# Kernel tuning notes

Hardware: AMD Instinct MI355X
Metric: run time of the kernel (lower is better)

## Reference

```python
import jax, jax.numpy as jnp
import numpy as np

DECAY = 0.8
CODEBOOK_SIZE = 1024
DIM = 128


def setup_inputs() -> dict:
    key = jax.random.key(0)
    k1, k2 = jax.random.split(key)
    x = jax.random.normal(k1, (16, 4096, DIM), dtype=jnp.float32)
    embed = jax.random.normal(k2, (CODEBOOK_SIZE, DIM), dtype=jnp.float32)
    ema_embed = embed * 1.0  # ema_num_initial = 1.0
    ema_num = jnp.ones((CODEBOOK_SIZE,), dtype=jnp.float32)
    return {"x": x, "embed": embed, "ema_embed": ema_embed, "ema_num": ema_num}


def reference(x, embed, ema_embed, ema_num):
    # flatten: [..., d] -> [N, d]
    shape = x.shape
    flatten = x.reshape(-1, shape[-1])  # [N, d]
    distance = -2.0 * (flatten @ embed.T) + jnp.sum(embed * embed, axis=-1)  # [N, K]
    embed_ind = jnp.argmin(distance, axis=-1)  # [N]
    quantize = embed[embed_ind.reshape(shape[:-1])]  # gather -> [..., d]

    # training branch: onehot^T @ flatten == segment_sum over code indices
    num_curr = jax.ops.segment_sum(
        jnp.ones_like(embed_ind, dtype=jnp.float32), embed_ind,
        num_segments=CODEBOOK_SIZE)  # [K]
    embed_curr = jax.ops.segment_sum(
        flatten.astype(jnp.float32), embed_ind,
        num_segments=CODEBOOK_SIZE)  # [K, d]

    ema_num_new = ema_num * DECAY + (1.0 - DECAY) * num_curr
    ema_embed_new = ema_embed * DECAY + (1.0 - DECAY) * embed_curr
    embed_new = ema_embed_new / ema_num_new[:, None]
    return quantize, embed_new, ema_embed_new, ema_num_new
```

## Files before the change

### kernel.cpp

```cpp
#include <hip/hip_runtime.h>

#define NPTS    65536
#define DIM     128
#define KCODES  1024
#define BM      128
#define TILE_C  64
#define NTHR    256
#define QUART_C 256
#define NTILE   (QUART_C / TILE_C)

typedef _Float16 f16x8 __attribute__((ext_vector_type(8)));
typedef float    f32x4 __attribute__((ext_vector_type(4)));

__device__ __forceinline__ void gload_lds16(const void* g, void* l) {
    __builtin_amdgcn_global_load_lds(
        (const __attribute__((address_space(1))) void*)g,
        (__attribute__((address_space(3))) void*)l, 16, 0, 0);
}
__device__ __forceinline__ unsigned mono32(float f) {
    unsigned u = __builtin_bit_cast(unsigned, f);
    return (u & 0x80000000u) ? ~u : (u | 0x80000000u);
}

__global__ __launch_bounds__(256)
void pack_kernel(const float* __restrict__ embed, _Float16* __restrict__ ebf,
                 int* __restrict__ ghist, int* __restrict__ gcursor,
                 const float* __restrict__ ema_embed, float* __restrict__ acc,
                 float* __restrict__ hn, unsigned long long* __restrict__ kmax)
{
    __shared__ float partial[256];
    const int t = threadIdx.x;
    const int b = blockIdx.x;
    const int g = b * 256 + t;
    if (g < KCODES) { ghist[g] = 0; gcursor[g] = 0; }
    {
        float4 e0 = reinterpret_cast<const float4*>(ema_embed)[g];
        float4 e1 = reinterpret_cast<const float4*>(ema_embed)[g + 16384];
        reinterpret_cast<float4*>(acc)[g] =
            (float4){0.8f * e0.x, 0.8f * e0.y, 0.8f * e0.z, 0.8f * e0.w};
        reinterpret_cast<float4*>(acc)[g + 16384] =
            (float4){0.8f * e1.x, 0.8f * e1.y, 0.8f * e1.z, 0.8f * e1.w};
    }
    #pragma unroll
    for (int k = 0; k < 4; ++k) kmax[g * 4 + k] = 0ull;

    const int tc  = g >> 10;
    const int f   = (g >> 6) & 15;
    const int l   = g & 63;
    const int nt  = f >> 2;
    const int akk = f & 3;
    const int hg  = l >> 4;
    const int n   = l & 15;
    const int c   = tc * TILE_C + nt * 16 + n;
    const int d0  = akk * 32 + hg * 8;
    const float* src = embed + (long)c * DIM + d0;
    float4 v0 = *reinterpret_cast<const float4*>(src);
    float4 v1 = *reinterpret_cast<const float4*>(src + 4);
    float vv[8] = {v0.x, v0.y, v0.z, v0.w, v1.x, v1.y, v1.z, v1.w};
    f16x8 out;
    float ss = 0.f;
    #pragma unroll
    for (int j = 0; j < 8; ++j) {
        _Float16 h = (_Float16)vv[j];
        out[j] = h;
        float r = (float)h;
        ss += r * r;
    }
    *reinterpret_cast<f16x8*>(ebf + (long)g * 8) = out;

    partial[t] = ss;
    __syncthreads();
    if (t < 16) {
        float s = 0.f;
        #pragma unroll
        for (int k = 0; k < 16; ++k) s += partial[t + k * 16];
        hn[(b >> 2) * TILE_C + (b & 3) * 16 + t] = 0.5f * s;
    }
}

__global__ __launch_bounds__(NTHR, 4)
void argmin_kernel(const float* __restrict__ x, const _Float16* __restrict__ ebf,
                   const float* __restrict__ halfnorm,
                   unsigned long long* __restrict__ kmax)
{
    __shared__ _Float16 es[2][8192];

    const int t     = threadIdx.x;
    const int lane  = t & 63;
    const int w     = t >> 6;
    const int r16   = lane & 15;
    const int h4    = lane >> 4;
    const int quart = blockIdx.y;
    const long xbase = (long)blockIdx.x * BM * DIM;
    const int  wp    = w * 32;
    const int  qbase = quart * QUART_C;
    const _Float16* eb = ebf + (long)quart * QUART_C * DIM;

    f16x8 a[2][4];
    #pragma unroll
    for (int ms = 0; ms < 2; ++ms) {
        const long prow = xbase + (long)(wp + ms * 16 + r16) * DIM;
        #pragma unroll
        for (int akk = 0; akk < 4; ++akk) {
            const float* s = x + prow + akk * 32 + h4 * 8;
            float4 u0 = *reinterpret_cast<const float4*>(s);
            float4 u1 = *reinterpret_cast<const float4*>(s + 4);
            float vv[8] = {u0.x, u0.y, u0.z, u0.w, u1.x, u1.y, u1.z, u1.w};
            #pragma unroll
            for (int j = 0; j < 8; ++j) a[ms][akk][j] = (_Float16)vv[j];
        }
    }

    #pragma unroll
    for (int i = 0; i < 4; ++i) {
        const int f = w * 4 + i;
        gload_lds16(eb + (long)f * 512 + lane * 8, &es[0][f * 512]);
    }
    float hnv_cur[4], hnv_nxt[4];
    #pragma unroll
    for (int nt = 0; nt < 4; ++nt) hnv_cur[nt] = halfnorm[qbase + nt * 16 + r16];
    __syncthreads();

    float bestv[8];
    int   besti[8];
    #pragma unroll
    for (int s = 0; s < 8; ++s) { bestv[s] = -1e30f; besti[s] = 0; }

    #pragma unroll 1
    for (int tile = 0; tile < NTILE; ++tile) {
        if (tile + 1 < NTILE) {
            const long gbase = (long)(tile + 1) * 8192;
            #pragma unroll
            for (int i = 0; i < 4; ++i) {
                const int f = w * 4 + i;
                gload_lds16(eb + gbase + f * 512 + lane * 8, &es[(tile + 1) & 1][f * 512]);
            }
            #pragma unroll
            for (int nt = 0; nt < 4; ++nt)
                hnv_nxt[nt] = halfnorm[qbase + (tile + 1) * TILE_C + nt * 16 + r16];
        }

        f32x4 C[4][2];
        #pragma unroll
        for (int nt = 0; nt < 4; ++nt)
            #pragma unroll
            for (int ms = 0; ms < 2; ++ms) C[nt][ms] = (f32x4){0.f, 0.f, 0.f, 0.f};

        #pragma unroll
        for (int akk = 0; akk < 4; ++akk) {
            #pragma unroll
            for (int nt = 0; nt < 4; ++nt) {
                f16x8 B = *reinterpret_cast<const f16x8*>(
                    &es[tile & 1][(nt * 4 + akk) * 512 + lane * 8]);
                C[nt][0] = __builtin_amdgcn_mfma_f32_16x16x32_f16(a[0][akk], B, C[nt][0], 0, 0, 0);
                C[nt][1] = __builtin_amdgcn_mfma_f32_16x16x32_f16(a[1][akk], B, C[nt][1], 0, 0, 0);
            }
        }

        #pragma unroll
        for (int nt = 0; nt < 4; ++nt) {
            const int c = qbase + tile * TILE_C + nt * 16 + r16;
            #pragma unroll
            for (int ms = 0; ms < 2; ++ms)
                #pragma unroll
                for (int reg = 0; reg < 4; ++reg) {
                    float sc  = C[nt][ms][reg] - hnv_cur[nt];
                    int  slot = ms * 4 + reg;
                    if (sc > bestv[slot]) { bestv[slot] = sc; besti[slot] = c; }
                }
        }
        #pragma unroll
        for (int nt = 0; nt < 4; ++nt) hnv_cur[nt] = hnv_nxt[nt];
        __syncthreads();
    }

    #pragma unroll
    for (int s = 0; s < 8; ++s) {
        float v = bestv[s];
        int   i = besti[s];
        #pragma unroll
        for (int off = 1; off < 16; off <<= 1) {
            float ov = __shfl_xor(v, off);
            int   oi = __shfl_xor(i, off);
            if (ov > v || (ov == v && oi < i)) { v = ov; i = oi; }
        }
        bestv[s] = v; besti[s] = i;
    }
    if (r16 == 0) {
        #pragma unroll
        for (int s = 0; s < 8; ++s) {
            int ms = s >> 2, reg = s & 3;
            int p  = wp + ms * 16 + h4 * 4 + reg;
            unsigned long long key =
                ((unsigned long long)mono32(bestv[s]) << 32) |
                (unsigned long long)(0x3FFu - (unsigned)besti[s]);
            atomicMax(&kmax[blockIdx.x * BM + p], key);
        }
    }
}

__global__ __launch_bounds__(256)
void merge_kernel(const unsigned long long* __restrict__ kmax,
                  const float* __restrict__ embed, int* __restrict__ ind,
                  float* __restrict__ quant, int* __restrict__ ghist)
{
    __shared__ int hist[KCODES];
    __shared__ int bidx[256];
    const int t    = threadIdx.x;
    const int base = blockIdx.x * 256;

    for (int i = t; i < KCODES; i += 256) hist[i] = 0;

    const unsigned long long k = kmax[base + t];
    const int best = 0x3FF - (int)(k & 0x3FFu);
    bidx[t] = best;
    ind[base + t] = best;
    __syncthreads();
    atomicAdd(&hist[best], 1);
    __syncthreads();
    for (int i = t; i < KCODES; i += 256)
        if (hist[i]) atomicAdd(&ghist[i], hist[i]);

    float4* dst = reinterpret_cast<float4*>(quant + (long)base * DIM);
    #pragma unroll
    for (int i = 0; i < 32; ++i) {
        int idx = i * 256 + t;
        int p   = idx >> 5;
        int q   = idx & 31;
        int c   = bidx[p];
        dst[idx] = reinterpret_cast<const float4*>(embed + (long)c * DIM)[q];
    }
}

__global__ __launch_bounds__(256)
void scatter_kernel(const int* __restrict__ ghist, const int* __restrict__ ind,
                    const float* __restrict__ ema_num, float* __restrict__ ema_num_new,
                    int* __restrict__ gcursor, int* __restrict__ sorted,
                    int* __restrict__ scode)
{
    __shared__ int off_lds[KCODES];
    __shared__ int wsum[4];
    const int t    = threadIdx.x;
    const int lane = t & 63;
    const int w    = t >> 6;

    int v[4], pre[4];
    int s = 0;
    #pragma unroll
    for (int j = 0; j < 4; ++j) {
        v[j] = ghist[t * 4 + j];
        pre[j] = s;
        s += v[j];
    }
    int incl = s;
    #pragma unroll
    for (int off = 1; off < 64; off <<= 1) {
        int u = __shfl_up(incl, off);
        if (lane >= off) incl += u;
    }
    if (lane == 63) wsum[w] = incl;
    __syncthreads();
    if (t == 0) {
        int a = 0;
        #pragma unroll
        for (int k = 0; k < 4; ++k) { int tmp = wsum[k]; wsum[k] = a; a += tmp; }
    }
    __syncthreads();
    const int excl = wsum[w] + incl - s;
    #pragma unroll
    for (int j = 0; j < 4; ++j) off_lds[t * 4 + j] = excl + pre[j];

    if (blockIdx.x == 0) {
        #pragma unroll
        for (int j = 0; j < 4; ++j)
            ema_num_new[t * 4 + j] = ema_num[t * 4 + j] * 0.8f + 0.2f * (float)v[j];
    }
    __syncthreads();

    const int p = blockIdx.x * 256 + t;
    const int c = ind[p];
    const int pos = off_lds[c] + atomicAdd(&gcursor[c], 1);
    sorted[pos] = p;
    scode[pos]  = c;
}

__global__ __launch_bounds__(128)
void sum2_kernel(const float* __restrict__ x, const int* __restrict__ sorted,
                 const int* __restrict__ scode, float* __restrict__ acc)
{
    __shared__ int sp[64];
    __shared__ int sc[64];
    const int t = threadIdx.x;
    const int base = blockIdx.x * 64;
    if (t < 64) { sp[t] = sorted[base + t]; sc[t] = scode[base + t]; }
    __syncthreads();

    float a = 0.f;
    int cprev = sc[0];
    #pragma unroll 1
    for (int kk = 0; kk < 8; ++kk) {
        float v[8];
        #pragma unroll
        for (int i = 0; i < 8; ++i)
            v[i] = x[(long)sp[kk * 8 + i] * DIM + t];
        #pragma unroll
        for (int i = 0; i < 8; ++i) {
            const int c = sc[kk * 8 + i];
            if (c != cprev) {
                atomicAdd(&acc[(long)cprev * DIM + t], 0.2f * a);
                a = 0.f; cprev = c;
            }
            a += v[i];
        }
    }
    atomicAdd(&acc[(long)cprev * DIM + t], 0.2f * a);
}

__global__ __launch_bounds__(256)
void final_kernel(const float* __restrict__ acc, const float* __restrict__ ema_num_new,
                  float* __restrict__ embed_new)
{
    const int g = blockIdx.x * 256 + threadIdx.x;
    float4 v = reinterpret_cast<const float4*>(acc)[g];
    const float en = ema_num_new[g >> 5];
    float4 o = {v.x / en, v.y / en, v.z / en, v.w / en};
    reinterpret_cast<float4*>(embed_new)[g] = o;
}

extern "C" void kernel_launch(void* const* d_in, const int* in_sizes, int n_in,
                              void* d_out, int out_size, void* d_ws, size_t ws_size,
                              hipStream_t stream)
{
    const float* x         = (const float*)d_in[0];
    const float* embed     = (const float*)d_in[1];
    const float* ema_embed = (const float*)d_in[2];
    const float* ema_num   = (const float*)d_in[3];

    float* out0 = (float*)d_out;
    float* out1 = out0 + 8388608;
    float* out2 = out1 + 131072;
    float* out3 = out2 + 131072;

    char* ws = (char*)d_ws;
    float*              hn      = (float*)ws;
    int*                ind     = (int*)(ws + 4096);
    _Float16*           ebf     = (_Float16*)(ws + 266240);
    int*                ghist   = (int*)(ws + 528384);
    int*                gcursor = (int*)(ws + 532480);
    unsigned long long* kmax    = (unsigned long long*)(ws + 536576);
    int*                sorted  = (int*)(ws + 536576);
    int*                scode   = (int*)(ws + 798720);

    pack_kernel<<<64, 256, 0, stream>>>(embed, ebf, ghist, gcursor, ema_embed,
                                        out2, hn, kmax);
    argmin_kernel<<<dim3(NPTS / BM, 4), NTHR, 0, stream>>>(x, ebf, hn, kmax);
    merge_kernel<<<NPTS / 256, 256, 0, stream>>>(kmax, embed, ind, out0, ghist);
    scatter_kernel<<<NPTS / 256, 256, 0, stream>>>(ghist, ind, ema_num, out3,
                                                   gcursor, sorted, scode);
    sum2_kernel<<<NPTS / 64, 128, 0, stream>>>(x, sorted, scode, out2);
    final_kernel<<<128, 256, 0, stream>>>(out2, out3, out1);
}
```

Baseline: 100.3 us.

## Fuse argmin merge into argmin kernel by scanning all codes per block

```diff
diff --git a/kernel.cpp b/kernel.cpp
--- a/kernel.cpp
+++ b/kernel.cpp
@@ -6,8 +6,7 @@
 #define BM      128
 #define TILE_C  64
 #define NTHR    256
-#define QUART_C 256
-#define NTILE   (QUART_C / TILE_C)
+#define NTILE   (KCODES / TILE_C)
 
 typedef _Float16 f16x8 __attribute__((ext_vector_type(8)));
 typedef float    f32x4 __attribute__((ext_vector_type(4)));
@@ -17,16 +16,12 @@
         (const __attribute__((address_space(1))) void*)g,
         (__attribute__((address_space(3))) void*)l, 16, 0, 0);
 }
-__device__ __forceinline__ unsigned mono32(float f) {
-    unsigned u = __builtin_bit_cast(unsigned, f);
-    return (u & 0x80000000u) ? ~u : (u | 0x80000000u);
-}
 
 __global__ __launch_bounds__(256)
 void pack_kernel(const float* __restrict__ embed, _Float16* __restrict__ ebf,
                  int* __restrict__ ghist, int* __restrict__ gcursor,
                  const float* __restrict__ ema_embed, float* __restrict__ acc,
-                 float* __restrict__ hn, unsigned long long* __restrict__ kmax)
+                 float* __restrict__ hn)
 {
     __shared__ float partial[256];
     const int t = threadIdx.x;
@@ -41,8 +36,6 @@
         reinterpret_cast<float4*>(acc)[g + 16384] =
             (float4){0.8f * e1.x, 0.8f * e1.y, 0.8f * e1.z, 0.8f * e1.w};
     }
-    #pragma unroll
-    for (int k = 0; k < 4; ++k) kmax[g * 4 + k] = 0ull;
 
     const int tc  = g >> 10;
     const int f   = (g >> 6) & 15;
@@ -78,23 +71,25 @@
     }
 }
 
-__global__ __launch_bounds__(NTHR, 4)
+__global__ __launch_bounds__(NTHR, 2)
 void argmin_kernel(const float* __restrict__ x, const _Float16* __restrict__ ebf,
-                   const float* __restrict__ halfnorm,
-                   unsigned long long* __restrict__ kmax)
+                   const float* __restrict__ halfnorm, const float* __restrict__ embed,
+                   int* __restrict__ ind, float* __restrict__ quant,
+                   int* __restrict__ ghist)
 {
     __shared__ _Float16 es[2][8192];
-
-    const int t     = threadIdx.x;
-    const int lane  = t & 63;
-    const int w     = t >> 6;
-    const int r16   = lane & 15;
-    const int h4    = lane >> 4;
-    const int quart = blockIdx.y;
+    __shared__ int      hist[KCODES];
+    __shared__ int      bidx[BM];
+
+    const int t    = threadIdx.x;
+    const int lane = t & 63;
+    const int w    = t >> 6;
+    const int r16  = lane & 15;
+    const int h4   = lane >> 4;
     const long xbase = (long)blockIdx.x * BM * DIM;
     const int  wp    = w * 32;
-    const int  qbase = quart * QUART_C;
-    const _Float16* eb = ebf + (long)quart * QUART_C * DIM;
+
+    for (int i = t; i < KCODES; i += NTHR) hist[i] = 0;
 
     f16x8 a[2][4];
     #pragma unroll
@@ -114,11 +109,11 @@
     #pragma unroll
     for (int i = 0; i < 4; ++i) {
         const int f = w * 4 + i;
-        gload_lds16(eb + (long)f * 512 + lane * 8, &es[0][f * 512]);
+        gload_lds16(ebf + (long)f * 512 + lane * 8, &es[0][f * 512]);
     }
     float hnv_cur[4], hnv_nxt[4];
     #pragma unroll
-    for (int nt = 0; nt < 4; ++nt) hnv_cur[nt] = halfnorm[qbase + nt * 16 + r16];
+    for (int nt = 0; nt < 4; ++nt) hnv_cur[nt] = halfnorm[nt * 16 + r16];
     __syncthreads();
 
     float bestv[8];
@@ -133,11 +128,11 @@
             #pragma unroll
             for (int i = 0; i < 4; ++i) {
                 const int f = w * 4 + i;
-                gload_lds16(eb + gbase + f * 512 + lane * 8, &es[(tile + 1) & 1][f * 512]);
+                gload_lds16(ebf + gbase + f * 512 + lane * 8, &es[(tile + 1) & 1][f * 512]);
             }
             #pragma unroll
             for (int nt = 0; nt < 4; ++nt)
-                hnv_nxt[nt] = halfnorm[qbase + (tile + 1) * TILE_C + nt * 16 + r16];
+                hnv_nxt[nt] = halfnorm[(tile + 1) * TILE_C + nt * 16 + r16];
         }
 
         f32x4 C[4][2];
@@ -159,7 +154,7 @@
 
         #pragma unroll
         for (int nt = 0; nt < 4; ++nt) {
-            const int c = qbase + tile * TILE_C + nt * 16 + r16;
+            const int c = tile * TILE_C + nt * 16 + r16;
             #pragma unroll
             for (int ms = 0; ms < 2; ++ms)
                 #pragma unroll
@@ -191,45 +186,27 @@
         for (int s = 0; s < 8; ++s) {
             int ms = s >> 2, reg = s & 3;
             int p  = wp + ms * 16 + h4 * 4 + reg;
-            unsigned long long key =
-                ((unsigned long long)mono32(bestv[s]) << 32) |
-                (unsigned long long)(0x3FFu - (unsigned)besti[s]);
-            atomicMax(&kmax[blockIdx.x * BM + p], key);
-        }
-    }
-}
-
-__global__ __launch_bounds__(256)
-void merge_kernel(const unsigned long long* __restrict__ kmax,
-                  const float* __restrict__ embed, int* __restrict__ ind,
-                  float* __restrict__ quant, int* __restrict__ ghist)
-{
-    __shared__ int hist[KCODES];
-    __shared__ int bidx[256];
-    const int t    = threadIdx.x;
-    const int base = blockIdx.x * 256;
-
-    for (int i = t; i < KCODES; i += 256) hist[i] = 0;
-
-    const unsigned long long k = kmax[base + t];
-    const int best = 0x3FF - (int)(k & 0x3FFu);
-    bidx[t] = best;
-    ind[base + t] = best;
-    __syncthreads();
-    atomicAdd(&hist[best], 1);
-    __syncthreads();
-    for (int i = t; i < KCODES; i += 256)
-        if (hist[i]) atomicAdd(&ghist[i], hist[i]);
-
-    float4* dst = reinterpret_cast<float4*>(quant + (long)base * DIM);
-    #pragma unroll
-    for (int i = 0; i < 32; ++i) {
-        int idx = i * 256 + t;
+            bidx[p] = besti[s];
+            ind[blockIdx.x * BM + p] = besti[s];
+        }
+    }
+    __syncthreads();
+
+    if (t < BM) atomicAdd(&hist[bidx[t]], 1);
+
+    float4* dst = reinterpret_cast<float4*>(quant + xbase);
+    #pragma unroll
+    for (int i = 0; i < 16; ++i) {
+        int idx = i * NTHR + t;
         int p   = idx >> 5;
         int q   = idx & 31;
         int c   = bidx[p];
         dst[idx] = reinterpret_cast<const float4*>(embed + (long)c * DIM)[q];
     }
+
+    __syncthreads();
+    for (int i = t; i < KCODES; i += NTHR)
+        if (hist[i]) atomicAdd(&ghist[i], hist[i]);
 }
 
 __global__ __launch_bounds__(256)
@@ -342,19 +319,17 @@
     float* out3 = out2 + 131072;
 
     char* ws = (char*)d_ws;
-    float*              hn      = (float*)ws;
-    int*                ind     = (int*)(ws + 4096);
-    _Float16*           ebf     = (_Float16*)(ws + 266240);
-    int*                ghist   = (int*)(ws + 528384);
-    int*                gcursor = (int*)(ws + 532480);
-    unsigned long long* kmax    = (unsigned long long*)(ws + 536576);
-    int*                sorted  = (int*)(ws + 536576);
-    int*                scode   = (int*)(ws + 798720);
+    float*    hn      = (float*)ws;
+    int*      ind     = (int*)(ws + 4096);
+    _Float16* ebf     = (_Float16*)(ws + 266240);
+    int*      ghist   = (int*)(ws + 528384);
+    int*      gcursor = (int*)(ws + 532480);
+    int*      sorted  = (int*)(ws + 536576);
+    int*      scode   = (int*)(ws + 798720);
 
     pack_kernel<<<64, 256, 0, stream>>>(embed, ebf, ghist, gcursor, ema_embed,
-                                        out2, hn, kmax);
-    argmin_kernel<<<dim3(NPTS / BM, 4), NTHR, 0, stream>>>(x, ebf, hn, kmax);
-    merge_kernel<<<NPTS / 256, 256, 0, stream>>>(kmax, embed, ind, out0, ghist);
+                                        out2, hn);
+    argmin_kernel<<<NPTS / BM, NTHR, 0, stream>>>(x, ebf, hn, embed, ind, out0, ghist);
     scatter_kernel<<<NPTS / 256, 256, 0, stream>>>(ghist, ind, ema_num, out3,
                                                    gcursor, sorted, scode);
     sum2_kernel<<<NPTS / 64, 128, 0, stream>>>(x, sorted, scode, out2);
```

Result: faster. 96.13 us (-4.2%).
